# Optimization experiments

Hardware: AMD Instinct MI355X
Metric: run time of the kernel (lower is better)

The kernel has to match this reference:

```python
import jax, jax.numpy as jnp
import numpy as np

N_NODES = 100000


def _gcn_layer(x, src, dst, deg_inv_sqrt, W, b):
    # GCNConv: out = D^{-1/2} (A + I) D^{-1/2} X W + b  (symmetric norm, self-loops)
    xw = x @ W  # [N, out]
    norm = deg_inv_sqrt[src] * deg_inv_sqrt[dst]  # [E]
    msg = xw[src] * norm[:, None]  # [E, out] gathered messages
    agg = jax.ops.segment_sum(msg, dst, num_segments=N_NODES)
    # self-loop contribution: norm_ii = deg_inv_sqrt[i]^2
    agg = agg + (deg_inv_sqrt * deg_inv_sqrt)[:, None] * xw
    return agg + b


def setup_inputs() -> dict:
    key = jax.random.key(0)
    k1, k2, k3, k4, k5, k6 = jax.random.split(key, 6)
    F_IN, HID, OUT, E = 128, 256, 40, 1600000
    x = jax.random.normal(k1, (N_NODES, F_IN), dtype=jnp.float32)
    edge_index = jax.random.randint(k2, (2, E), 0, N_NODES, dtype=jnp.int64)
    s1 = 1.0 / np.sqrt(F_IN)
    s2 = 1.0 / np.sqrt(HID)
    W1 = jax.random.uniform(k3, (F_IN, HID), jnp.float32, -s1, s1)
    b1 = jnp.zeros((HID,), jnp.float32)
    W2 = jax.random.uniform(k4, (HID, OUT), jnp.float32, -s2, s2)
    b2 = jnp.zeros((OUT,), jnp.float32)
    return {"x": x, "edge_index": edge_index, "W1": W1, "b1": b1, "W2": W2, "b2": b2}


def reference(x, edge_index, W1, b1, W2, b2):
    src, dst = edge_index[0], edge_index[1]
    # degree with self-loops (GCNConv default add_self_loops=True)
    deg = jax.ops.segment_sum(jnp.ones_like(dst, dtype=x.dtype), dst, num_segments=N_NODES) + 1.0
    deg_inv_sqrt = jax.lax.rsqrt(deg)
    h = _gcn_layer(x, src, dst, deg_inv_sqrt, W1, b1)
    h = jax.nn.relu(h)
    # dropout is identity in eval mode
    h = _gcn_layer(h, src, dst, deg_inv_sqrt, W2, b2)
    return jax.nn.log_softmax(h, axis=1)
```

## Files before the change

kernel.cpp:

```cpp
#include <hip/hip_runtime.h>
#include <math.h>

typedef long long ll;
typedef unsigned int uint;
typedef __attribute__((ext_vector_type(8))) short bf16x8;
typedef __attribute__((ext_vector_type(4))) float f32x4;

#define FIN 128
#define HID 256
#define FOUT 40
#define NG 8

__device__ __forceinline__ float bflo(uint u) { return __uint_as_float(u << 16); }
__device__ __forceinline__ float bfhi(uint u) { return __uint_as_float(u & 0xFFFF0000u); }
__device__ __forceinline__ unsigned short f2bf(float f) {
  uint u = __float_as_uint(f);
  u += 0x7FFFu + ((u >> 16) & 1u);
  return (unsigned short)(u >> 16);
}

__device__ __forceinline__ int detect64(const uint* __restrict__ ei) {
  return (ei[1] == 0u && ei[3] == 0u && ei[5] == 0u && ei[7] == 0u) ? 1 : 0;
}

__global__ __launch_bounds__(256) void k_init(
    const void* __restrict__ ei, int* __restrict__ cnt,
    const float* __restrict__ W1, const float* __restrict__ W2,
    unsigned short* __restrict__ w1p, unsigned short* __restrict__ w2p,
    int2* __restrict__ pairs, int n, ll E) {
  int i = blockIdx.x * 256 + threadIdx.x;
  int T = gridDim.x * 256;
  if (i < n) cnt[i] = 0;
  if (i < 32768) {
    int j = i & 7, g = (i >> 3) & 3, c = (i >> 5) & 255, s = i >> 13;
    int k = s * 32 + g * 8 + j;
    w1p[i] = f2bf(W1[(size_t)k * HID + c]);
  } else if (i < 32768 + 12288) {
    int i2 = i - 32768;
    int j = i2 & 7, g = (i2 >> 3) & 3, q = i2 >> 5;
    int c = q % 48, s = q / 48;
    int k = s * 32 + g * 8 + j;
    w2p[i2] = (c < FOUT) ? f2bf(W2[(size_t)k * FOUT + c]) : (unsigned short)0;
  }
  int is64 = detect64((const uint*)ei);
  for (ll base = (ll)i * 4; base < E; base += (ll)T * 4) {
    int m = (int)((E - base < 4) ? (E - base) : 4);
    int s[4], d[4];
    if (is64) {
      if (m == 4) {
        longlong2 a0 = *(const longlong2*)((const ll*)ei + base);
        longlong2 a1 = *(const longlong2*)((const ll*)ei + base + 2);
        longlong2 b0 = *(const longlong2*)((const ll*)ei + E + base);
        longlong2 b1 = *(const longlong2*)((const ll*)ei + E + base + 2);
        s[0]=(int)a0.x; s[1]=(int)a0.y; s[2]=(int)a1.x; s[3]=(int)a1.y;
        d[0]=(int)b0.x; d[1]=(int)b0.y; d[2]=(int)b1.x; d[3]=(int)b1.y;
      } else {
        for (int j = 0; j < m; ++j) { s[j]=(int)((const ll*)ei)[base+j]; d[j]=(int)((const ll*)ei)[E+base+j]; }
      }
    } else {
      if (m == 4) {
        int4 a = *(const int4*)((const int*)ei + base);
        int4 b = *(const int4*)((const int*)ei + E + base);
        s[0]=a.x; s[1]=a.y; s[2]=a.z; s[3]=a.w;
        d[0]=b.x; d[1]=b.y; d[2]=b.z; d[3]=b.w;
      } else {
        for (int j = 0; j < m; ++j) { s[j]=((const int*)ei)[base+j]; d[j]=((const int*)ei)[E+base+j]; }
      }
    }
    for (int j = 0; j < m; ++j) pairs[base + j] = make_int2(s[j], d[j]);
  }
}

__global__ __launch_bounds__(256) void k_count(
    const int2* __restrict__ pairs, int* __restrict__ cnt, ll E, int range, int n) {
  int g = blockIdx.x & (NG - 1);
  int lo = g * range;
  int hi = min(n, lo + range);
  ll tig = (ll)(blockIdx.x >> 3) * 256 + threadIdx.x;
  ll TIG = (ll)(gridDim.x >> 3) * 256;
  for (ll i = tig * 2; i < E; i += TIG * 2) {
    if (i + 1 < E) {
      int4 p = *(const int4*)(pairs + i);
      if (p.y >= lo && p.y < hi) atomicAdd(&cnt[p.y], 1);
      if (p.w >= lo && p.w < hi) atomicAdd(&cnt[p.w], 1);
    } else {
      int2 p = pairs[i];
      if (p.y >= lo && p.y < hi) atomicAdd(&cnt[p.y], 1);
    }
  }
}

__global__ __launch_bounds__(1024) void k_scan1(const int* __restrict__ cnt,
                                                int* __restrict__ row_off,
                                                int* __restrict__ blksums, int n) {
  __shared__ int sm[1024];
  int t = threadIdx.x;
  int base = blockIdx.x * 4096 + t * 4;
  int v0 = (base + 0 < n) ? cnt[base + 0] : 0;
  int v1 = (base + 1 < n) ? cnt[base + 1] : 0;
  int v2 = (base + 2 < n) ? cnt[base + 2] : 0;
  int v3 = (base + 3 < n) ? cnt[base + 3] : 0;
  int s = v0 + v1 + v2 + v3;
  sm[t] = s;
  __syncthreads();
  for (int off = 1; off < 1024; off <<= 1) {
    int u = (t >= off) ? sm[t - off] : 0;
    __syncthreads();
    sm[t] += u;
    __syncthreads();
  }
  int excl = sm[t] - s;
  if (base + 0 < n) row_off[base + 0] = excl;
  if (base + 1 < n) row_off[base + 1] = excl + v0;
  if (base + 2 < n) row_off[base + 2] = excl + v0 + v1;
  if (base + 3 < n) row_off[base + 3] = excl + v0 + v1 + v2;
  if (t == 1023) blksums[blockIdx.x] = sm[1023];
}

__global__ void k_scan2(int* __restrict__ blksums, int nb) {
  if (threadIdx.x == 0 && blockIdx.x == 0) {
    int acc = 0;
    for (int i = 0; i < nb; ++i) { int v = blksums[i]; blksums[i] = acc; acc += v; }
    blksums[nb] = acc;
  }
}

__global__ void k_scan3(int* __restrict__ row_off, int* __restrict__ cursor,
                        const int* __restrict__ blksums, float* __restrict__ dis,
                        int n, int nb) {
  int i = blockIdx.x * 1024 + threadIdx.x;
  if (i < n) {
    int c = cursor[i];
    int v = row_off[i] + blksums[i >> 12];
    row_off[i] = v;
    cursor[i] = v;
    dis[i] = rsqrtf((float)c + 1.0f);
  }
  if (i == 0) row_off[n] = blksums[nb];
}

__global__ __launch_bounds__(256) void k_fill(
    const int2* __restrict__ pairs, int* __restrict__ cursor,
    int* __restrict__ csr, ll E, int range, int n) {
  int g = blockIdx.x & (NG - 1);
  int lo = g * range;
  int hi = min(n, lo + range);
  ll tig = (ll)(blockIdx.x >> 3) * 256 + threadIdx.x;
  ll TIG = (ll)(gridDim.x >> 3) * 256;
  for (ll i = tig * 2; i < E; i += TIG * 2) {
    if (i + 1 < E) {
      int4 p = *(const int4*)(pairs + i);
      if (p.y >= lo && p.y < hi) { int pos = atomicAdd(&cursor[p.y], 1); csr[pos] = p.x; }
      if (p.w >= lo && p.w < hi) { int pos = atomicAdd(&cursor[p.w], 1); csr[pos] = p.z; }
    } else {
      int2 p = pairs[i];
      if (p.y >= lo && p.y < hi) { int pos = atomicAdd(&cursor[p.y], 1); csr[pos] = p.x; }
    }
  }
}

__global__ __launch_bounds__(256) void k_xcast(
    const float* __restrict__ x, const float* __restrict__ dis,
    unsigned short* __restrict__ xb, int total8) {
  int i = blockIdx.x * 256 + threadIdx.x;
  if (i >= total8) return;
  float w = dis[i >> 4];
  const float4* p = (const float4*)x + (size_t)i * 2;
  float4 a = p[0], b = p[1];
  uint4 o;
  o.x = (uint)f2bf(w * a.x) | ((uint)f2bf(w * a.y) << 16);
  o.y = (uint)f2bf(w * a.z) | ((uint)f2bf(w * a.w) << 16);
  o.z = (uint)f2bf(w * b.x) | ((uint)f2bf(w * b.y) << 16);
  o.w = (uint)f2bf(w * b.z) | ((uint)f2bf(w * b.w) << 16);
  *(uint4*)(xb + (size_t)i * 8) = o;
}

__device__ __forceinline__ void add8(float* a, uint4 r) {
  a[0] += bflo(r.x); a[1] += bfhi(r.x);
  a[2] += bflo(r.y); a[3] += bfhi(r.y);
  a[4] += bflo(r.z); a[5] += bfhi(r.z);
  a[6] += bflo(r.w); a[7] += bfhi(r.w);
}

__global__ __launch_bounds__(256) void k_fused1(
    const unsigned short* __restrict__ xb, const int* __restrict__ csr,
    const int* __restrict__ row_off, const float* __restrict__ dis,
    const unsigned short* __restrict__ w1p, const float* __restrict__ b1,
    const unsigned short* __restrict__ w2p, unsigned short* __restrict__ xw2b,
    int n)
{
  __shared__ __align__(16) unsigned short xsb[16 * 136];
  __shared__ __align__(16) unsigned short hsb[16 * 264];

  int tid = threadIdx.x;
  int n0 = blockIdx.x * 16;
  int wv = tid >> 6, lane = tid & 63, qq = lane >> 4, l16 = lane & 15;
  int nl = wv * 4 + qq;
  int node = n0 + nl;

  float a[8] = {0, 0, 0, 0, 0, 0, 0, 0};
  float di = 0.f;
  if (node < n) {
    di = dis[node];
    uint4 v = *((const uint4*)(xb + (size_t)node * FIN) + l16);
    add8(a, v);
    int e0 = row_off[node], e1 = row_off[node + 1];
    int e = e0;
    for (; e + 8 <= e1; e += 8) {
      int s0 = csr[e],     s1 = csr[e + 1], s2 = csr[e + 2], s3 = csr[e + 3];
      int s4 = csr[e + 4], s5 = csr[e + 5], s6 = csr[e + 6], s7 = csr[e + 7];
      uint4 r0 = *((const uint4*)(xb + (size_t)s0 * FIN) + l16);
      uint4 r1 = *((const uint4*)(xb + (size_t)s1 * FIN) + l16);
      uint4 r2 = *((const uint4*)(xb + (size_t)s2 * FIN) + l16);
      uint4 r3 = *((const uint4*)(xb + (size_t)s3 * FIN) + l16);
      uint4 r4 = *((const uint4*)(xb + (size_t)s4 * FIN) + l16);
      uint4 r5 = *((const uint4*)(xb + (size_t)s5 * FIN) + l16);
      uint4 r6 = *((const uint4*)(xb + (size_t)s6 * FIN) + l16);
      uint4 r7 = *((const uint4*)(xb + (size_t)s7 * FIN) + l16);
      add8(a, r0); add8(a, r1); add8(a, r2); add8(a, r3);
      add8(a, r4); add8(a, r5); add8(a, r6); add8(a, r7);
    }
    for (; e < e1; ++e) {
      uint4 r0 = *((const uint4*)(xb + (size_t)csr[e] * FIN) + l16);
      add8(a, r0);
    }
  }
  {
    uint4 pk;
    pk.x = (uint)f2bf(di * a[0]) | ((uint)f2bf(di * a[1]) << 16);
    pk.y = (uint)f2bf(di * a[2]) | ((uint)f2bf(di * a[3]) << 16);
    pk.z = (uint)f2bf(di * a[4]) | ((uint)f2bf(di * a[5]) << 16);
    pk.w = (uint)f2bf(di * a[6]) | ((uint)f2bf(di * a[7]) << 16);
    *(uint4*)(xsb + nl * 136 + l16 * 8) = pk;
  }
  __syncthreads();

  int mrow = lane & 15, g = lane >> 4;
  f32x4 acc1[4] = {{0,0,0,0},{0,0,0,0},{0,0,0,0},{0,0,0,0}};
  #pragma unroll
  for (int s = 0; s < 4; ++s) {
    bf16x8 av = *(const bf16x8*)(xsb + mrow * 136 + s * 32 + g * 8);
    #pragma unroll
    for (int t = 0; t < 4; ++t) {
      int c = wv * 64 + t * 16 + mrow;
      bf16x8 bv = *(const bf16x8*)(w1p + (((size_t)(s * 256 + c) * 4 + g) << 3));
      acc1[t] = __builtin_amdgcn_mfma_f32_16x16x32_bf16(av, bv, acc1[t], 0, 0, 0);
    }
  }
  #pragma unroll
  for (int t = 0; t < 4; ++t) {
    int c = wv * 64 + t * 16 + mrow;
    float bb = b1[c];
    #pragma unroll
    for (int r = 0; r < 4; ++r) {
      float v = fmaxf(acc1[t][r] + bb, 0.f);
      hsb[(g * 4 + r) * 264 + c] = f2bf(v);
    }
  }
  __syncthreads();

  if (wv < 3) {
    f32x4 acc2 = {0, 0, 0, 0};
    int c2 = wv * 16 + mrow;
    #pragma unroll
    for (int s = 0; s < 8; ++s) {
      bf16x8 av = *(const bf16x8*)(hsb + mrow * 264 + s * 32 + g * 8);
      bf16x8 bv = *(const bf16x8*)(w2p + (((size_t)(s * 48 + c2) * 4 + g) << 3));
      acc2 = __builtin_amdgcn_mfma_f32_16x16x32_bf16(av, bv, acc2, 0, 0, 0);
    }
    if (c2 < FOUT) {
      #pragma unroll
      for (int r = 0; r < 4; ++r) {
        int nodeg = n0 + g * 4 + r;
        if (nodeg < n)
          xw2b[((size_t)nodeg << 6) + c2] = f2bf(acc2[r] * dis[nodeg]);
      }
    }
  }
}

__global__ __launch_bounds__(256) void k_layer2(
    const unsigned short* __restrict__ xw2b, const int* __restrict__ csr,
    const int* __restrict__ row_off, const float* __restrict__ dis,
    const float* __restrict__ b2, float* __restrict__ out, int n)
{
  int tid = threadIdx.x;
  int node = blockIdx.x * 16 + (tid >> 4);
  int l16 = tid & 15;
  if (node >= n) return;
  float di = dis[node];
  float a0, a1, a2, a3;
  {
    uint2 v = *((const uint2*)(xw2b + ((size_t)node << 6)) + l16);
    a0 = bflo(v.x); a1 = bfhi(v.x); a2 = bflo(v.y); a3 = bfhi(v.y);
  }
  int e0 = row_off[node], e1 = row_off[node + 1];
  int e = e0;
  for (; e + 8 <= e1; e += 8) {
    int s0 = csr[e],     s1 = csr[e + 1], s2 = csr[e + 2], s3 = csr[e + 3];
    int s4 = csr[e + 4], s5 = csr[e + 5], s6 = csr[e + 6], s7 = csr[e + 7];
    uint2 r0 = *((const uint2*)(xw2b + ((size_t)s0 << 6)) + l16);
    uint2 r1 = *((const uint2*)(xw2b + ((size_t)s1 << 6)) + l16);
    uint2 r2 = *((const uint2*)(xw2b + ((size_t)s2 << 6)) + l16);
    uint2 r3 = *((const uint2*)(xw2b + ((size_t)s3 << 6)) + l16);
    uint2 r4 = *((const uint2*)(xw2b + ((size_t)s4 << 6)) + l16);
    uint2 r5 = *((const uint2*)(xw2b + ((size_t)s5 << 6)) + l16);
    uint2 r6 = *((const uint2*)(xw2b + ((size_t)s6 << 6)) + l16);
    uint2 r7 = *((const uint2*)(xw2b + ((size_t)s7 << 6)) + l16);
    a0 += bflo(r0.x); a1 += bfhi(r0.x); a2 += bflo(r0.y); a3 += bfhi(r0.y);
    a0 += bflo(r1.x); a1 += bfhi(r1.x); a2 += bflo(r1.y); a3 += bfhi(r1.y);
    a0 += bflo(r2.x); a1 += bfhi(r2.x); a2 += bflo(r2.y); a3 += bfhi(r2.y);
    a0 += bflo(r3.x); a1 += bfhi(r3.x); a2 += bflo(r3.y); a3 += bfhi(r3.y);
    a0 += bflo(r4.x); a1 += bfhi(r4.x); a2 += bflo(r4.y); a3 += bfhi(r4.y);
    a0 += bflo(r5.x); a1 += bfhi(r5.x); a2 += bflo(r5.y); a3 += bfhi(r5.y);
    a0 += bflo(r6.x); a1 += bfhi(r6.x); a2 += bflo(r6.y); a3 += bfhi(r6.y);
    a0 += bflo(r7.x); a1 += bfhi(r7.x); a2 += bflo(r7.y); a3 += bfhi(r7.y);
  }
  for (; e < e1; ++e) {
    uint2 r0 = *((const uint2*)(xw2b + ((size_t)csr[e] << 6)) + l16);
    a0 += bflo(r0.x); a1 += bfhi(r0.x); a2 += bflo(r0.y); a3 += bfhi(r0.y);
  }
  bool act = (l16 < 10);
  float l0 = -INFINITY, l1 = -INFINITY, l2 = -INFINITY, l3 = -INFINITY;
  if (act) {
    float4 bv = *(const float4*)(b2 + l16 * 4);
    l0 = di * a0 + bv.x; l1 = di * a1 + bv.y;
    l2 = di * a2 + bv.z; l3 = di * a3 + bv.w;
  }
  float m = fmaxf(fmaxf(l0, l1), fmaxf(l2, l3));
  #pragma unroll
  for (int off = 8; off > 0; off >>= 1) m = fmaxf(m, __shfl_xor(m, off));
  float s = 0.f;
  if (act) s = expf(l0 - m) + expf(l1 - m) + expf(l2 - m) + expf(l3 - m);
  #pragma unroll
  for (int off = 8; off > 0; off >>= 1) s += __shfl_xor(s, off);
  if (act) {
    float ls = m + logf(s);
    float4 o = make_float4(l0 - ls, l1 - ls, l2 - ls, l3 - ls);
    *(float4*)(out + (size_t)node * FOUT + l16 * 4) = o;
  }
}

extern "C" void kernel_launch(void* const* d_in, const int* in_sizes, int n_in,
                              void* d_out, int out_size, void* d_ws, size_t ws_size,
                              hipStream_t stream) {
  const float* x  = (const float*)d_in[0];
  const void*  ei = d_in[1];
  const float* W1 = (const float*)d_in[2];
  const float* b1 = (const float*)d_in[3];
  const float* W2 = (const float*)d_in[4];
  const float* b2 = (const float*)d_in[5];
  float* out = (float*)d_out;

  int n = in_sizes[0] / FIN;
  ll  E = (ll)in_sizes[1] / 2;
  int nb = (n + 4095) / 4096;
  int range = (n + NG - 1) / NG;

  char* ws = (char*)d_ws;
  size_t off = 0;
  auto carve = [&](size_t bytes) -> char* {
    char* p = ws + off;
    off = (off + bytes + 255) & ~(size_t)255;
    return p;
  };
  int*   row_off = (int*)carve((size_t)(n + 1) * 4);
  int*   cursor  = (int*)carve((size_t)n * 4);
  int2*  pairs   = (int2*)carve((size_t)E * 8);
  int*   csr     = (int*)carve((size_t)E * 4);
  int*   blksums = (int*)carve(64 * 4);
  float* dis     = (float*)carve((size_t)n * 4);
  unsigned short* xb   = (unsigned short*)carve((size_t)n * FIN * 2);
  unsigned short* w1p  = (unsigned short*)carve(32768 * 2);
  unsigned short* w2p  = (unsigned short*)carve(12288 * 2);
  unsigned short* xw2b = (unsigned short*)carve((size_t)n * 64 * 2);
  (void)n_in; (void)out_size; (void)ws_size;

  int gn256 = (n + 255) / 256;
  int gx8   = (n * FIN / 8 + 255) / 256;
  int gt16  = (n + 15) / 16;

  hipLaunchKernelGGL(k_init,  dim3(gn256), dim3(256), 0, stream,
                     ei, cursor, W1, W2, w1p, w2p, pairs, n, E);
  hipLaunchKernelGGL(k_count, dim3(512), dim3(256), 0, stream, pairs, cursor, E, range, n);
  hipLaunchKernelGGL(k_scan1, dim3(nb), dim3(1024), 0, stream, cursor, row_off, blksums, n);
  hipLaunchKernelGGL(k_scan2, dim3(1), dim3(1), 0, stream, blksums, nb);
  hipLaunchKernelGGL(k_scan3, dim3((n + 1023) / 1024), dim3(1024), 0, stream,
                     row_off, cursor, blksums, dis, n, nb);
  hipLaunchKernelGGL(k_fill,  dim3(512), dim3(256), 0, stream, pairs, cursor, csr, E, range, n);
  hipLaunchKernelGGL(k_xcast, dim3(gx8), dim3(256), 0, stream, x, dis, xb, n * FIN / 8);
  hipLaunchKernelGGL(k_fused1, dim3(gt16), dim3(256), 0, stream,
                     xb, csr, row_off, dis, w1p, b1, w2p, xw2b, n);
  hipLaunchKernelGGL(k_layer2, dim3(gt16), dim3(256), 0, stream,
                     xw2b, csr, row_off, dis, b2, out, n);
}
```

Measured before the change: 313.9 us.

## Process nodes in degree-sorted order to balance per-wavefront gather work

Builds a permutation of nodes bucketed by in-degree (a histogram in scan3, a prefix kernel, and a per-block counting-sort kernel), then has the fused layer-1 and layer-2 kernels process nodes in that order. Nodes sharing a wavefront and block then have similar edge counts, which reduces divergence and tail imbalance in the CSR gather loops. The cost is two extra kernel launches, a perm indirection, and scattered output writes. Reading nodes out of natural order may also reduce locality.

```diff
diff --git a/kernel.cpp b/kernel.cpp
--- a/kernel.cpp
+++ b/kernel.cpp
@@ -10,6 +10,7 @@
 #define HID 256
 #define FOUT 40
 #define NG 8
+#define NBIN 64
 
 __device__ __forceinline__ float bflo(uint u) { return __uint_as_float(u << 16); }
 __device__ __forceinline__ float bfhi(uint u) { return __uint_as_float(u & 0xFFFF0000u); }
@@ -27,10 +28,11 @@
     const void* __restrict__ ei, int* __restrict__ cnt,
     const float* __restrict__ W1, const float* __restrict__ W2,
     unsigned short* __restrict__ w1p, unsigned short* __restrict__ w2p,
-    int2* __restrict__ pairs, int n, ll E) {
+    int2* __restrict__ pairs, int* __restrict__ hist, int n, ll E) {
   int i = blockIdx.x * 256 + threadIdx.x;
   int T = gridDim.x * 256;
   if (i < n) cnt[i] = 0;
+  if (i < NBIN) hist[i] = 0;
   if (i < 32768) {
     int j = i & 7, g = (i >> 3) & 3, c = (i >> 5) & 255, s = i >> 13;
     int k = s * 32 + g * 8 + j;
@@ -125,18 +127,65 @@
   }
 }
 
-__global__ void k_scan3(int* __restrict__ row_off, int* __restrict__ cursor,
-                        const int* __restrict__ blksums, float* __restrict__ dis,
-                        int n, int nb) {
-  int i = blockIdx.x * 1024 + threadIdx.x;
+__global__ __launch_bounds__(1024) void k_scan3(
+    int* __restrict__ row_off, int* __restrict__ cursor,
+    const int* __restrict__ blksums, float* __restrict__ dis,
+    int* __restrict__ hist, int n, int nb) {
+  __shared__ int lh[NBIN];
+  int t = threadIdx.x;
+  if (t < NBIN) lh[t] = 0;
+  __syncthreads();
+  int i = blockIdx.x * 1024 + t;
   if (i < n) {
     int c = cursor[i];
     int v = row_off[i] + blksums[i >> 12];
     row_off[i] = v;
     cursor[i] = v;
     dis[i] = rsqrtf((float)c + 1.0f);
+    atomicAdd(&lh[min(c, NBIN - 1)], 1);
   }
   if (i == 0) row_off[n] = blksums[nb];
+  __syncthreads();
+  if (t < NBIN && lh[t]) atomicAdd(&hist[t], lh[t]);
+}
+
+__global__ void k_binpfx(const int* __restrict__ hist, int* __restrict__ bincur) {
+  if (threadIdx.x == 0 && blockIdx.x == 0) {
+    int acc = 0;
+    for (int b = 0; b < NBIN; ++b) { int v = hist[b]; bincur[b] = acc; acc += v; }
+  }
+}
+
+__global__ __launch_bounds__(256) void k_perm(
+    const int* __restrict__ row_off, int* __restrict__ bincur,
+    int* __restrict__ perm, int n) {
+  __shared__ int lh[NBIN], lbase[NBIN];
+  int t = threadIdx.x;
+  if (t < NBIN) lh[t] = 0;
+  __syncthreads();
+  int base = blockIdx.x * 4096 + t * 16;
+  int deg[16];
+  #pragma unroll
+  for (int j = 0; j < 16; ++j) {
+    int i = base + j;
+    if (i < n) {
+      deg[j] = min(row_off[i + 1] - row_off[i], NBIN - 1);
+      atomicAdd(&lh[deg[j]], 1);
+    } else deg[j] = -1;
+  }
+  __syncthreads();
+  if (t < NBIN) {
+    lbase[t] = lh[t] ? atomicAdd(&bincur[t], lh[t]) : 0;
+    lh[t] = 0;
+  }
+  __syncthreads();
+  #pragma unroll
+  for (int j = 0; j < 16; ++j) {
+    if (deg[j] >= 0) {
+      int r = atomicAdd(&lh[deg[j]], 1);
+      perm[lbase[deg[j]] + r] = base + j;
+    }
+  }
 }
 
 __global__ __launch_bounds__(256) void k_fill(
@@ -185,22 +234,26 @@
 __global__ __launch_bounds__(256) void k_fused1(
     const unsigned short* __restrict__ xb, const int* __restrict__ csr,
     const int* __restrict__ row_off, const float* __restrict__ dis,
+    const int* __restrict__ perm,
     const unsigned short* __restrict__ w1p, const float* __restrict__ b1,
     const unsigned short* __restrict__ w2p, unsigned short* __restrict__ xw2b,
     int n)
 {
   __shared__ __align__(16) unsigned short xsb[16 * 136];
   __shared__ __align__(16) unsigned short hsb[16 * 264];
+  __shared__ int   nid[16];
+  __shared__ float dsh[16];
 
   int tid = threadIdx.x;
   int n0 = blockIdx.x * 16;
   int wv = tid >> 6, lane = tid & 63, qq = lane >> 4, l16 = lane & 15;
   int nl = wv * 4 + qq;
-  int node = n0 + nl;
+  int idx = n0 + nl;
+  int node = (idx < n) ? perm[idx] : -1;
 
   float a[8] = {0, 0, 0, 0, 0, 0, 0, 0};
   float di = 0.f;
-  if (node < n) {
+  if (node >= 0) {
     di = dis[node];
     uint4 v = *((const uint4*)(xb + (size_t)node * FIN) + l16);
     add8(a, v);
@@ -225,6 +278,7 @@
       add8(a, r0);
     }
   }
+  if (l16 == 0) { nid[nl] = node; dsh[nl] = di; }
   {
     uint4 pk;
     pk.x = (uint)f2bf(di * a[0]) | ((uint)f2bf(di * a[1]) << 16);
@@ -271,9 +325,9 @@
     if (c2 < FOUT) {
       #pragma unroll
       for (int r = 0; r < 4; ++r) {
-        int nodeg = n0 + g * 4 + r;
-        if (nodeg < n)
-          xw2b[((size_t)nodeg << 6) + c2] = f2bf(acc2[r] * dis[nodeg]);
+        int nodeg = nid[g * 4 + r];
+        if (nodeg >= 0)
+          xw2b[((size_t)nodeg << 6) + c2] = f2bf(acc2[r] * dsh[g * 4 + r]);
       }
     }
   }
@@ -282,12 +336,14 @@
 __global__ __launch_bounds__(256) void k_layer2(
     const unsigned short* __restrict__ xw2b, const int* __restrict__ csr,
     const int* __restrict__ row_off, const float* __restrict__ dis,
+    const int* __restrict__ perm,
     const float* __restrict__ b2, float* __restrict__ out, int n)
 {
   int tid = threadIdx.x;
-  int node = blockIdx.x * 16 + (tid >> 4);
+  int idx = blockIdx.x * 16 + (tid >> 4);
   int l16 = tid & 15;
-  if (node >= n) return;
+  if (idx >= n) return;
+  int node = perm[idx];
   float di = dis[node];
   float a0, a1, a2, a3;
   {
@@ -369,6 +425,9 @@
   int2*  pairs   = (int2*)carve((size_t)E * 8);
   int*   csr     = (int*)carve((size_t)E * 4);
   int*   blksums = (int*)carve(64 * 4);
+  int*   hist    = (int*)carve(NBIN * 4);
+  int*   bincur  = (int*)carve(NBIN * 4);
+  int*   perm    = (int*)carve((size_t)n * 4);
   float* dis     = (float*)carve((size_t)n * 4);
   unsigned short* xb   = (unsigned short*)carve((size_t)n * FIN * 2);
   unsigned short* w1p  = (unsigned short*)carve(32768 * 2);
@@ -379,18 +438,21 @@
   int gn256 = (n + 255) / 256;
   int gx8   = (n * FIN / 8 + 255) / 256;
   int gt16  = (n + 15) / 16;
+  int gperm = (n + 4095) / 4096;
 
   hipLaunchKernelGGL(k_init,  dim3(gn256), dim3(256), 0, stream,
-                     ei, cursor, W1, W2, w1p, w2p, pairs, n, E);
+                     ei, cursor, W1, W2, w1p, w2p, pairs, hist, n, E);
   hipLaunchKernelGGL(k_count, dim3(512), dim3(256), 0, stream, pairs, cursor, E, range, n);
   hipLaunchKernelGGL(k_scan1, dim3(nb), dim3(1024), 0, stream, cursor, row_off, blksums, n);
   hipLaunchKernelGGL(k_scan2, dim3(1), dim3(1), 0, stream, blksums, nb);
   hipLaunchKernelGGL(k_scan3, dim3((n + 1023) / 1024), dim3(1024), 0, stream,
-                     row_off, cursor, blksums, dis, n, nb);
+                     row_off, cursor, blksums, dis, hist, n, nb);
+  hipLaunchKernelGGL(k_binpfx, dim3(1), dim3(1), 0, stream, hist, bincur);
+  hipLaunchKernelGGL(k_perm,  dim3(gperm), dim3(256), 0, stream, row_off, bincur, perm, n);
   hipLaunchKernelGGL(k_fill,  dim3(512), dim3(256), 0, stream, pairs, cursor, csr, E, range, n);
   hipLaunchKernelGGL(k_xcast, dim3(gx8), dim3(256), 0, stream, x, dis, xb, n * FIN / 8);
   hipLaunchKernelGGL(k_fused1, dim3(gt16), dim3(256), 0, stream,
-                     xb, csr, row_off, dis, w1p, b1, w2p, xw2b, n);
+                     xb, csr, row_off, dis, perm, w1p, b1, w2p, xw2b, n);
   hipLaunchKernelGGL(k_layer2, dim3(gt16), dim3(256), 0, stream,
-                     xw2b, csr, row_off, dis, b2, out, n);
-}
+                     xw2b, csr, row_off, dis, perm, b2, out, n);
+}
```

Result: faster. 302.3 us (-3.7%).
